# Kernel optimization log

Measured on AMD Instinct MI355X. Metric: run time of the kernel, lower is better.

The kernel has to match this reference:

```python
import jax, jax.numpy as jnp
import numpy as np

SINKHORN_ITERS = 5
EPS_CLAMP = 1e-8   # matches torch eps=1e-08 in unbalanced_optimal_transport
EPS_COS = 1e-6     # matches cosine_distance eps
EPS_DIV = 1e-6     # matches weighted_ref / rigid transform eps


def setup_inputs() -> dict:
    key = jax.random.key(0)
    k0, k1, k2, k3 = jax.random.split(key, 4)
    B, D, M, N = 32, 512, 1024, 1024
    return {
        "src_embedding": jax.random.normal(k0, (B, D, M), dtype=jnp.float32),
        "tgt_embedding": jax.random.normal(k1, (B, D, N), dtype=jnp.float32),
        "src": jax.random.normal(k2, (B, 3, M), dtype=jnp.float32),
        "tgt": jax.random.normal(k3, (B, 3, N), dtype=jnp.float32),
        "l": jnp.float32(1.0),    # learned scalar nn.Parameter
        "rho": jnp.float32(1.0),  # learned scalar nn.Parameter
    }


def reference(src_embedding, tgt_embedding, src, tgt, l, rho):
    # ---- batched cosine distance: C[b] = 1 - <x1, x2> / (|x1||x2|) ----
    x1 = jnp.swapaxes(src_embedding, 1, 2)  # (B, M, D)
    x2 = jnp.swapaxes(tgt_embedding, 1, 2)  # (B, N, D)
    w1 = jnp.linalg.norm(x1, axis=2, keepdims=True)  # (B, M, 1)
    w2 = jnp.linalg.norm(x2, axis=2, keepdims=True)  # (B, N, 1)
    denom = jnp.clip(w1 * jnp.swapaxes(w2, 1, 2), EPS_COS, None)
    C = 1.0 - jnp.einsum('bmd,bnd->bmn', x1, x2) / denom  # (B, M, N)

    # ---- batched unbalanced Sinkhorn (5 fixed iterations) ----
    B, M, N = C.shape
    a = jnp.float32(1.0 / M)
    b = jnp.float32(1.0 / N)
    K = jnp.exp(-C / jnp.clip(l, EPS_CLAMP, None))        # (B, M, N)
    fi = rho / jnp.clip(rho + l, EPS_CLAMP, None)
    v = jnp.full((B, N), b, dtype=C.dtype)
    u = jnp.full((B, M), a, dtype=C.dtype)
    for _ in range(SINKHORN_ITERS):
        u = (a / jnp.clip(jnp.einsum('bmn,bn->bm', K, v), EPS_CLAMP, None)) ** fi
        v = (b / jnp.clip(jnp.einsum('bmn,bm->bn', K, u), EPS_CLAMP, None)) ** fi
    P = u[:, :, None] * K * v[:, None, :]                  # transport plan (B, M, N)

    # ---- soft correspondences ----
    row = jnp.sum(P, axis=2)                               # (B, M)
    tgt_pts = jnp.swapaxes(tgt, 1, 2)                      # (B, N, 3)
    weighted_ref = jnp.einsum('bmn,bnd->bmd', P, tgt_pts) / (row[:, :, None] + EPS_DIV)

    # ---- weighted Kabsch rigid transform (batched 3x3 SVD) ----
    a_pts = jnp.swapaxes(src, 1, 2)                        # (B, M, 3)
    w = row[:, :, None] / (jnp.sum(row, axis=1)[:, None, None] + EPS_DIV)  # (B, M, 1)
    centroid_a = jnp.sum(a_pts * w, axis=1)                # (B, 3)
    centroid_b = jnp.sum(weighted_ref * w, axis=1)         # (B, 3)
    a_c = a_pts - centroid_a[:, None, :]
    b_c = weighted_ref - centroid_b[:, None, :]
    cov = jnp.einsum('bmi,bmj->bij', a_c, b_c * w)         # (B, 3, 3)

    U, S, Vh = jnp.linalg.svd(cov, full_matrices=True)
    V = jnp.swapaxes(Vh, 1, 2)                             # torch.svd returns V, not V^T
    Ut = jnp.swapaxes(U, 1, 2)
    rot_pos = V @ Ut
    rot_neg = V.at[:, :, 2].multiply(-1.0) @ Ut            # flip last column of V
    det = jnp.linalg.det(rot_pos)[:, None, None]
    R = jnp.where(det > 0, rot_pos, rot_neg)               # (B, 3, 3)
    t = -jnp.einsum('bij,bj->bi', R, centroid_a) + centroid_b  # (B, 3)
    return R, t, P
```

## Files before the change

### kernel.cpp

```cpp
#include <hip/hip_runtime.h>
#include <math.h>

#define BB 32
#define DD 512
#define MM 1024
#define NN 1024

typedef float f32x4 __attribute__((ext_vector_type(4)));
typedef _Float16 f16x8 __attribute__((ext_vector_type(8)));


__global__ __launch_bounds__(256)
void prep_kernel(const float* __restrict__ srcE, const float* __restrict__ tgtE,
                 float* __restrict__ w1, float* __restrict__ w2,
                 float* __restrict__ v, float* __restrict__ colsum,
                 float* __restrict__ Pout)
{
    __shared__ float T[64][65];
    __shared__ float nsum[64];
    const int mc  = blockIdx.x;
    const int mat = blockIdx.y;
    const int b   = blockIdx.z;
    const int tid = threadIdx.x;
    const float* E = mat ? tgtE : srcE;
    float* w = mat ? w2 : w1;

    if (tid < 64) nsum[tid] = 0.f;
    if (mat == 0 && tid < 64) {
        const int idx = ((b << 4) + mc) * 64 + tid;
        v[idx] = 1.0f / 1024.0f;
        colsum[idx] = 0.0f;
    }

    const int m4  = (tid & 15) * 4;
    const int din = tid >> 4;
    const int m0g = mc * 64;
    const float* Eb = E + (size_t)b * (DD * MM) + m0g;

    const int row = tid >> 2;
    const int dc4 = tid & 3;
    const int Rrow = mat * 32768 + b * 1024 + m0g + row;
    char* obase = (char*)Pout + (((size_t)(Rrow >> 1)) << 12) + 2048
                + ((size_t)(Rrow & 1) << 10);

    float nacc[4] = {0.f, 0.f, 0.f, 0.f};

    for (int p = 0; p < 8; ++p) {
        const int d0 = p * 64;
        __syncthreads();
        float4 ld[4];
        #pragma unroll
        for (int s = 0; s < 4; ++s) {
            const int d = d0 + din + 16 * s;
            ld[s] = *reinterpret_cast<const float4*>(Eb + (size_t)d * MM + m4);
        }
        #pragma unroll
        for (int s = 0; s < 4; ++s) {
            nacc[0] = fmaf(ld[s].x, ld[s].x, nacc[0]);
            nacc[1] = fmaf(ld[s].y, ld[s].y, nacc[1]);
            nacc[2] = fmaf(ld[s].z, ld[s].z, nacc[2]);
            nacc[3] = fmaf(ld[s].w, ld[s].w, nacc[3]);
            *reinterpret_cast<float4*>(&T[din + 16 * s][m4]) = ld[s];
        }
        __syncthreads();
        __attribute__((aligned(16))) _Float16 h[16];
        #pragma unroll
        for (int k = 0; k < 16; ++k) h[k] = (_Float16)T[dc4 * 16 + k][row];
        *reinterpret_cast<f16x8*>(obase + (size_t)(d0 + dc4 * 16) * 2)
            = *reinterpret_cast<f16x8*>(&h[0]);
        *reinterpret_cast<f16x8*>(obase + (size_t)(d0 + dc4 * 16 + 8) * 2)
            = *reinterpret_cast<f16x8*>(&h[8]);
    }
    #pragma unroll
    for (int q = 0; q < 4; ++q) atomicAdd(&nsum[m4 + q], nacc[q]);
    __syncthreads();
    if (tid < 64) w[b * 1024 + m0g + tid] = sqrtf(nsum[tid]);
}

__global__ __launch_bounds__(256)
void gemm_kexp_kernel(const float* __restrict__ w1, const float* __restrict__ w2,
                      const float* __restrict__ lp, float* __restrict__ Kout)
{
    __shared__ _Float16 As[2][8192];
    __shared__ _Float16 Bs[2][8192];

    const int tid  = threadIdx.x;
    const int lane = tid & 63;
    const int wave = tid >> 6;
    const int m0 = blockIdx.x * 128;
    const int n0 = blockIdx.y * 128;
    const int b  = blockIdx.z;
    const int wm = (wave & 1) * 64;
    const int wn = (wave >> 1) * 64;
    const int m16  = lane & 15;
    const int quad = lane >> 4;

    const char* pbase = (const char*)Kout;
    const char* srcA[4]; const char* srcB[4];
    #pragma unroll
    for (int c = 0; c < 4; ++c) {
        const int idx  = (wave * 4 + c) * 64 + lane;
        const int m    = idx >> 3;
        const int kg   = idx & 7;
        const int colb = ((kg ^ (m & 7)) << 4);
        const int Ra = b * 1024 + m0 + m;
        srcA[c] = pbase + (((size_t)(Ra >> 1)) << 12) + 2048
                + ((size_t)(Ra & 1) << 10) + colb;
        const int Rb = 32768 + b * 1024 + n0 + m;
        srcB[c] = pbase + (((size_t)(Rb >> 1)) << 12) + 2048
                + ((size_t)(Rb & 1) << 10) + colb;
    }

    f32x4 acc[4][4];
    #pragma unroll
    for (int i = 0; i < 4; ++i)
        #pragma unroll
        for (int j = 0; j < 4; ++j)
            acc[i][j] = (f32x4){0.f, 0.f, 0.f, 0.f};

    auto stage = [&](int buf, int kt_) {
        const int kb = kt_ * 128;
        #pragma unroll
        for (int c = 0; c < 4; ++c) {
            __builtin_amdgcn_global_load_lds(
                (const __attribute__((address_space(1))) unsigned int*)(srcA[c] + kb),
                (__attribute__((address_space(3))) unsigned int*)&As[buf][(wave * 4 + c) * 512],
                16, 0, 0);
            __builtin_amdgcn_global_load_lds(
                (const __attribute__((address_space(1))) unsigned int*)(srcB[c] + kb),
                (__attribute__((address_space(3))) unsigned int*)&Bs[buf][(wave * 4 + c) * 512],
                16, 0, 0);
        }
    };

    stage(0, 0);
    __syncthreads();
    int cur = 0;
    for (int kt = 0; kt < 8; ++kt) {
        if (kt < 7) stage(cur ^ 1, kt + 1);
        #pragma unroll
        for (int ks = 0; ks < 2; ++ks) {
            const int kg = ks * 4 + quad;
            f16x8 af[4], bfr[4];
            #pragma unroll
            for (int i = 0; i < 4; ++i) {
                const int rm = wm + i * 16 + m16;
                af[i]  = *reinterpret_cast<const f16x8*>(&As[cur][rm * 64 + ((kg ^ (rm & 7)) << 3)]);
                const int rn = wn + i * 16 + m16;
                bfr[i] = *reinterpret_cast<const f16x8*>(&Bs[cur][rn * 64 + ((kg ^ (rn & 7)) << 3)]);
            }
            #pragma unroll
            for (int i = 0; i < 4; ++i)
                #pragma unroll
                for (int j = 0; j < 4; ++j)
                    acc[i][j] = __builtin_amdgcn_mfma_f32_16x16x32_f16(af[i], bfr[j], acc[i][j], 0, 0, 0);
        }
        __syncthreads();
        cur ^= 1;
    }

    const float inv_l = 1.0f / fmaxf(lp[0], 1e-8f);
    float w2v[4];
    #pragma unroll
    for (int j = 0; j < 4; ++j) w2v[j] = w2[b * NN + n0 + wn + j * 16 + m16];
    unsigned short* Ls = (unsigned short*)&As[0][0];
    #pragma unroll
    for (int i = 0; i < 4; ++i) {
        #pragma unroll
        for (int r = 0; r < 4; ++r) {
            const int m = wm + i * 16 + quad * 4 + r;
            const float w1v = w1[b * MM + m0 + m];
            #pragma unroll
            for (int j = 0; j < 4; ++j) {
                const float dot = acc[i][j][r];
                const float den = fmaxf(w1v * w2v[j], 1e-6f);
                const float kv  = __expf((dot / den - 1.0f) * inv_l);
                const int n = wn + j * 16 + m16;
                const int sidx = m * 128 + ((((n >> 3) ^ (m & 7)) << 3) | (n & 7));
                Ls[sidx] = (unsigned short)fminf(fmaf(kv, 65535.0f, 0.5f), 65535.0f);
            }
        }
    }
    __syncthreads();
    const int row = tid >> 1, half = tid & 1;
    char* orow = (char*)Kout + ((size_t)(b * 1024 + m0 + row) << 12)
               + (size_t)n0 * 2 + half * 128;
    #pragma unroll
    for (int c = 0; c < 8; ++c) {
        const int g = half * 8 + c;
        const uint4 val = *reinterpret_cast<const uint4*>(
            &Ls[row * 128 + ((g ^ (row & 7)) << 3)]);
        reinterpret_cast<uint4*>(orow)[c] = val;
    }
}

__global__ __launch_bounds__(256)
void uv_fused_kernel(const float* __restrict__ Kmat, const float* __restrict__ v,
                     float* __restrict__ u, float* __restrict__ colsum,
                     const float* __restrict__ lp, const float* __restrict__ rp)
{
    const int ms = blockIdx.x;
    const int b  = blockIdx.y;
    const int wv = threadIdx.x >> 6, lane = threadIdx.x & 63;
    const float l = lp[0], rho = rp[0];
    const float fi = rho / fmaxf(rho + l, 1e-8f);
    const int m0 = ms * 32 + wv * 8;
    const int gid0 = (b << 10) + m0;

    uint4 ku[8][2];
    #pragma unroll
    for (int r = 0; r < 8; ++r) {
        const uint4* kr = (const uint4*)((const char*)Kmat + ((size_t)(gid0 + r) << 12));
        ku[r][0] = kr[lane];
        ku[r][1] = kr[64 + lane];
    }
    const float4* vb4 = (const float4*)(v + (b << 10));
    float4 vv[4];
    vv[0] = vb4[2 * lane];       vv[1] = vb4[2 * lane + 1];
    vv[2] = vb4[128 + 2 * lane]; vv[3] = vb4[129 + 2 * lane];

    float s[8];
    #pragma unroll
    for (int r = 0; r < 8; ++r) {
        float t = 0.f;
        #pragma unroll
        for (int c = 0; c < 2; ++c) {
            const uint4 q = ku[r][c];
            const float4 va = vv[2 * c], vb2 = vv[2 * c + 1];
            t = fmaf((float)(q.x & 0xffffu), va.x, t);
            t = fmaf((float)(q.x >> 16),     va.y, t);
            t = fmaf((float)(q.y & 0xffffu), va.z, t);
            t = fmaf((float)(q.y >> 16),     va.w, t);
            t = fmaf((float)(q.z & 0xffffu), vb2.x, t);
            t = fmaf((float)(q.z >> 16),     vb2.y, t);
            t = fmaf((float)(q.w & 0xffffu), vb2.z, t);
            t = fmaf((float)(q.w >> 16),     vb2.w, t);
        }
        s[r] = t;
    }
    #pragma unroll
    for (int off = 32; off > 0; off >>= 1)
        #pragma unroll
        for (int r = 0; r < 8; ++r) s[r] += __shfl_down(s[r], off);
    float um[8];
    #pragma unroll
    for (int r = 0; r < 8; ++r) {
        const float sv = __builtin_amdgcn_readfirstlane(s[r]) * (1.0f / 65535.0f);
        um[r] = __powf((1.0f / 1024.0f) / fmaxf(sv, 1e-8f), fi);
    }
    if (lane == 0) {
        float* ub = u + (b << 10);
        #pragma unroll
        for (int r = 0; r < 8; ++r) ub[m0 + r] = um[r];
    }

    float cacc[16];
    #pragma unroll
    for (int j = 0; j < 16; ++j) cacc[j] = 0.f;
    #pragma unroll
    for (int r = 0; r < 8; ++r) {
        const float umr = um[r];
        #pragma unroll
        for (int c = 0; c < 2; ++c) {
            const uint4 q = ku[r][c];
            float* cc = &cacc[8 * c];
            cc[0] = fmaf((float)(q.x & 0xffffu), umr, cc[0]);
            cc[1] = fmaf((float)(q.x >> 16),     umr, cc[1]);
            cc[2] = fmaf((float)(q.y & 0xffffu), umr, cc[2]);
            cc[3] = fmaf((float)(q.y >> 16),     umr, cc[3]);
            cc[4] = fmaf((float)(q.z & 0xffffu), umr, cc[4]);
            cc[5] = fmaf((float)(q.z >> 16),     umr, cc[5]);
            cc[6] = fmaf((float)(q.w & 0xffffu), umr, cc[6]);
            cc[7] = fmaf((float)(q.w >> 16),     umr, cc[7]);
        }
    }
    __shared__ float red[4][1024];
    *reinterpret_cast<float4*>(&red[wv][8 * lane])           = make_float4(cacc[0],  cacc[1],  cacc[2],  cacc[3]);
    *reinterpret_cast<float4*>(&red[wv][8 * lane + 4])       = make_float4(cacc[4],  cacc[5],  cacc[6],  cacc[7]);
    *reinterpret_cast<float4*>(&red[wv][512 + 8 * lane])     = make_float4(cacc[8],  cacc[9],  cacc[10], cacc[11]);
    *reinterpret_cast<float4*>(&red[wv][512 + 8 * lane + 4]) = make_float4(cacc[12], cacc[13], cacc[14], cacc[15]);
    __syncthreads();
    const int t = threadIdx.x;
    float4 s4 = *reinterpret_cast<const float4*>(&red[0][4 * t]);
    #pragma unroll
    for (int w = 1; w < 4; ++w) {
        const float4 rw = *reinterpret_cast<const float4*>(&red[w][4 * t]);
        s4.x += rw.x; s4.y += rw.y; s4.z += rw.z; s4.w += rw.w;
    }
    float* cs = colsum + (b << 10) + 4 * t;
    atomicAdd(cs + 0, s4.x);
    atomicAdd(cs + 1, s4.y);
    atomicAdd(cs + 2, s4.z);
    atomicAdd(cs + 3, s4.w);
}

__global__ __launch_bounds__(256)
void v_finalize_kernel(float* __restrict__ colsum, float* __restrict__ v,
                       const float* __restrict__ lp, const float* __restrict__ rp)
{
    const int idx = blockIdx.x * 256 + threadIdx.x;
    const float s = colsum[idx] * (1.0f / 65535.0f);
    colsum[idx] = 0.0f;
    const float l = lp[0], rho = rp[0];
    const float fi = rho / fmaxf(rho + l, 1e-8f);
    v[idx] = __powf((1.0f / 1024.0f) / fmaxf(s, 1e-8f), fi);
}

__global__ __launch_bounds__(256)
void p_pass_kernel(float* __restrict__ Kmat, const float* __restrict__ u,
                   const float* __restrict__ v, const float* __restrict__ tgt,
                   float* __restrict__ rowb, float* __restrict__ wref)
{
    const int gid  = (blockIdx.x * 256 + threadIdx.x) >> 6;
    const int lane = threadIdx.x & 63;
    const int b = gid >> 10;
    char* rowbase = (char*)Kmat + ((size_t)gid << 12);
    const uint4* kr = (const uint4*)rowbase;
    uint4 ku[2];
    ku[0] = kr[lane];
    ku[1] = kr[64 + lane];
    const float4* vb = (const float4*)(v + (b << 10));
    const float4* tb = (const float4*)(tgt + (size_t)b * 3072);
    const float um_s = u[gid] * (1.0f / 65535.0f);
    float4 vv[4], txa[4], tya[4], tza[4];
    vv[0]  = vb[2 * lane];        vv[1]  = vb[2 * lane + 1];
    vv[2]  = vb[128 + 2 * lane];  vv[3]  = vb[129 + 2 * lane];
    txa[0] = tb[2 * lane];        txa[1] = tb[2 * lane + 1];
    txa[2] = tb[128 + 2 * lane];  txa[3] = tb[129 + 2 * lane];
    tya[0] = tb[256 + 2 * lane];  tya[1] = tb[257 + 2 * lane];
    tya[2] = tb[384 + 2 * lane];  tya[3] = tb[385 + 2 * lane];
    tza[0] = tb[512 + 2 * lane];  tza[1] = tb[513 + 2 * lane];
    tza[2] = tb[640 + 2 * lane];  tza[3] = tb[641 + 2 * lane];
    asm volatile("s_waitcnt vmcnt(0)" ::: "memory");
    float4* prow = (float4*)rowbase;
    float s = 0.f, x = 0.f, y = 0.f, z = 0.f;
    #pragma unroll
    for (int c = 0; c < 2; ++c) {
        const uint4 q = ku[c];
        const float k0 = (float)(q.x & 0xffffu), k1 = (float)(q.x >> 16);
        const float k2 = (float)(q.y & 0xffffu), k3 = (float)(q.y >> 16);
        const float k4 = (float)(q.z & 0xffffu), k5 = (float)(q.z >> 16);
        const float k6 = (float)(q.w & 0xffffu), k7 = (float)(q.w >> 16);
        const float4 va = vv[2 * c], vb2 = vv[2 * c + 1];
        float4 pa, pb;
        pa.x = um_s * k0 * va.x;  pa.y = um_s * k1 * va.y;
        pa.z = um_s * k2 * va.z;  pa.w = um_s * k3 * va.w;
        pb.x = um_s * k4 * vb2.x; pb.y = um_s * k5 * vb2.y;
        pb.z = um_s * k6 * vb2.z; pb.w = um_s * k7 * vb2.w;
        prow[c * 128 + 2 * lane]     = pa;
        prow[c * 128 + 2 * lane + 1] = pb;
        s += (pa.x + pa.y) + (pa.z + pa.w) + (pb.x + pb.y) + (pb.z + pb.w);
        const float4 x0 = txa[2 * c], x1 = txa[2 * c + 1];
        const float4 y0 = tya[2 * c], y1 = tya[2 * c + 1];
        const float4 z0 = tza[2 * c], z1 = tza[2 * c + 1];
        x = fmaf(pa.x, x0.x, x); x = fmaf(pa.y, x0.y, x);
        x = fmaf(pa.z, x0.z, x); x = fmaf(pa.w, x0.w, x);
        x = fmaf(pb.x, x1.x, x); x = fmaf(pb.y, x1.y, x);
        x = fmaf(pb.z, x1.z, x); x = fmaf(pb.w, x1.w, x);
        y = fmaf(pa.x, y0.x, y); y = fmaf(pa.y, y0.y, y);
        y = fmaf(pa.z, y0.z, y); y = fmaf(pa.w, y0.w, y);
        y = fmaf(pb.x, y1.x, y); y = fmaf(pb.y, y1.y, y);
        y = fmaf(pb.z, y1.z, y); y = fmaf(pb.w, y1.w, y);
        z = fmaf(pa.x, z0.x, z); z = fmaf(pa.y, z0.y, z);
        z = fmaf(pa.z, z0.z, z); z = fmaf(pa.w, z0.w, z);
        z = fmaf(pb.x, z1.x, z); z = fmaf(pb.y, z1.y, z);
        z = fmaf(pb.z, z1.z, z); z = fmaf(pb.w, z1.w, z);
    }
    #pragma unroll
    for (int off = 32; off > 0; off >>= 1) {
        s += __shfl_down(s, off);
        x += __shfl_down(x, off);
        y += __shfl_down(y, off);
        z += __shfl_down(z, off);
    }
    if (lane == 0) {
        rowb[gid] = s;
        const float inv = 1.0f / (s + 1e-6f);
        wref[gid * 3 + 0] = x * inv;
        wref[gid * 3 + 1] = y * inv;
        wref[gid * 3 + 2] = z * inv;
    }
}

__device__ __forceinline__ float block_reduce_sum(float x, float* lds4, int wv, int lane)
{
    #pragma unroll
    for (int off = 32; off > 0; off >>= 1) x += __shfl_down(x, off);
    __syncthreads();
    if (lane == 0) lds4[wv] = x;
    __syncthreads();
    return (lds4[0] + lds4[1]) + (lds4[2] + lds4[3]);
}

__global__ __launch_bounds__(256)
void kabsch_stats_kernel(const float* __restrict__ rowb, const float* __restrict__ wref,
                         const float* __restrict__ src, float* __restrict__ cov,
                         float* __restrict__ ca, float* __restrict__ cb)
{
    __shared__ float lds4[4];
    const int b = blockIdx.x, tid = threadIdx.x;
    const int wv = tid >> 6, lane = tid & 63;
    float r[4], w[4], ax[4], ay[4], az[4], bx[4], by[4], bz[4];
    float rsum = 0.f;
    #pragma unroll
    for (int i = 0; i < 4; ++i) {
        const int m = tid + 256 * i;
        r[i] = rowb[(b << 10) + m];
        rsum += r[i];
    }
    const float total = block_reduce_sum(rsum, lds4, wv, lane);
    const float inv = 1.0f / (total + 1e-6f);
    #pragma unroll
    for (int i = 0; i < 4; ++i) {
        const int m = tid + 256 * i;
        w[i]  = r[i] * inv;
        ax[i] = src[b * 3072 + m];
        ay[i] = src[b * 3072 + 1024 + m];
        az[i] = src[b * 3072 + 2048 + m];
        bx[i] = wref[((b << 10) + m) * 3 + 0];
        by[i] = wref[((b << 10) + m) * 3 + 1];
        bz[i] = wref[((b << 10) + m) * 3 + 2];
    }
    float cax = 0, cay = 0, caz = 0, cbx = 0, cby = 0, cbz = 0;
    #pragma unroll
    for (int i = 0; i < 4; ++i) {
        cax = fmaf(ax[i], w[i], cax); cay = fmaf(ay[i], w[i], cay); caz = fmaf(az[i], w[i], caz);
        cbx = fmaf(bx[i], w[i], cbx); cby = fmaf(by[i], w[i], cby); cbz = fmaf(bz[i], w[i], cbz);
    }
    cax = block_reduce_sum(cax, lds4, wv, lane);
    cay = block_reduce_sum(cay, lds4, wv, lane);
    caz = block_reduce_sum(caz, lds4, wv, lane);
    cbx = block_reduce_sum(cbx, lds4, wv, lane);
    cby = block_reduce_sum(cby, lds4, wv, lane);
    cbz = block_reduce_sum(cbz, lds4, wv, lane);
    float c[9] = {0,0,0,0,0,0,0,0,0};
    #pragma unroll
    for (int i = 0; i < 4; ++i) {
        const float dax = ax[i] - cax, day = ay[i] - cay, daz = az[i] - caz;
        const float dbx = (bx[i] - cbx) * w[i];
        const float dby = (by[i] - cby) * w[i];
        const float dbz = (bz[i] - cbz) * w[i];
        c[0] = fmaf(dax, dbx, c[0]); c[1] = fmaf(dax, dby, c[1]); c[2] = fmaf(dax, dbz, c[2]);
        c[3] = fmaf(day, dbx, c[3]); c[4] = fmaf(day, dby, c[4]); c[5] = fmaf(day, dbz, c[5]);
        c[6] = fmaf(daz, dbx, c[6]); c[7] = fmaf(daz, dby, c[7]); c[8] = fmaf(daz, dbz, c[8]);
    }
    #pragma unroll
    for (int k = 0; k < 9; ++k) c[k] = block_reduce_sum(c[k], lds4, wv, lane);
    if (tid == 0) {
        #pragma unroll
        for (int k = 0; k < 9; ++k) cov[b * 9 + k] = c[k];
        ca[b * 3 + 0] = cax; ca[b * 3 + 1] = cay; ca[b * 3 + 2] = caz;
        cb[b * 3 + 0] = cbx; cb[b * 3 + 1] = cby; cb[b * 3 + 2] = cbz;
    }
}

__device__ __forceinline__ void jrot_d(double S[3][3], double V[3][3], int p, int q)
{
    const double apq = S[p][q];
    if (fabs(apq) < 1e-300) return;
    const double theta = (S[q][q] - S[p][p]) / (2.0 * apq);
    const double tt = copysign(1.0, theta) / (fabs(theta) + sqrt(1.0 + theta * theta));
    const double c = 1.0 / sqrt(1.0 + tt * tt);
    const double s = tt * c;
    #pragma unroll
    for (int k = 0; k < 3; ++k) {
        const double skp = S[k][p], skq = S[k][q];
        S[k][p] = c * skp - s * skq;
        S[k][q] = s * skp + c * skq;
    }
    #pragma unroll
    for (int k = 0; k < 3; ++k) {
        const double spk = S[p][k], sqk = S[q][k];
        S[p][k] = c * spk - s * sqk;
        S[q][k] = s * spk + c * sqk;
    }
    #pragma unroll
    for (int k = 0; k < 3; ++k) {
        const double vkp = V[k][p], vkq = V[k][q];
        V[k][p] = c * vkp - s * vkq;
        V[k][q] = s * vkp + c * vkq;
    }
}

__global__ __launch_bounds__(64)
void svd_kernel(const float* __restrict__ cov, const float* __restrict__ ca,
                const float* __restrict__ cb, float* __restrict__ out)
{
    const int b = threadIdx.x;
    if (b >= 32) return;
    double A[3][3];
    #pragma unroll
    for (int i = 0; i < 3; ++i)
        #pragma unroll
        for (int j = 0; j < 3; ++j)
            A[i][j] = (double)cov[b * 9 + i * 3 + j];
    double S[3][3];
    #pragma unroll
    for (int i = 0; i < 3; ++i)
        #pragma unroll
        for (int j = 0; j < 3; ++j)
            S[i][j] = A[0][i] * A[0][j] + A[1][i] * A[1][j] + A[2][i] * A[2][j];
    double V[3][3] = {{1,0,0},{0,1,0},{0,0,1}};
    for (int sweep = 0; sweep < 8; ++sweep) {
        jrot_d(S, V, 0, 1);
        jrot_d(S, V, 0, 2);
        jrot_d(S, V, 1, 2);
    }
    int o0 = 0, o1 = 1, o2 = 2;
    double e0 = S[0][0], e1 = S[1][1], e2 = S[2][2];
    double tf; int ti;
    if (e0 < e1) { tf = e0; e0 = e1; e1 = tf; ti = o0; o0 = o1; o1 = ti; }
    if (e0 < e2) { tf = e0; e0 = e2; e2 = tf; ti = o0; o0 = o2; o2 = ti; }
    if (e1 < e2) { tf = e1; e1 = e2; e2 = tf; ti = o1; o1 = o2; o2 = ti; }
    double v1[3] = {V[0][o0], V[1][o0], V[2][o0]};
    double v2[3] = {V[0][o1], V[1][o1], V[2][o1]};
    double v3[3] = {V[0][o2], V[1][o2], V[2][o2]};
    double Av1[3], Av2[3];
    #pragma unroll
    for (int i = 0; i < 3; ++i) {
        Av1[i] = A[i][0] * v1[0] + A[i][1] * v1[1] + A[i][2] * v1[2];
        Av2[i] = A[i][0] * v2[0] + A[i][1] * v2[1] + A[i][2] * v2[2];
    }
    const double n1 = sqrt(Av1[0]*Av1[0] + Av1[1]*Av1[1] + Av1[2]*Av1[2]);
    const double in1 = 1.0 / fmax(n1, 1e-300);
    double u1[3] = {Av1[0]*in1, Av1[1]*in1, Av1[2]*in1};
    const double d12 = Av2[0]*u1[0] + Av2[1]*u1[1] + Av2[2]*u1[2];
    double u2[3] = {Av2[0] - d12*u1[0], Av2[1] - d12*u1[1], Av2[2] - d12*u1[2]};
    const double n2 = sqrt(u2[0]*u2[0] + u2[1]*u2[1] + u2[2]*u2[2]);
    const double in2 = 1.0 / fmax(n2, 1e-300);
    u2[0] *= in2; u2[1] *= in2; u2[2] *= in2;
    double u3[3] = {u1[1]*u2[2] - u1[2]*u2[1],
                    u1[2]*u2[0] - u1[0]*u2[2],
                    u1[0]*u2[1] - u1[1]*u2[0]};
    double R0[3][3];
    #pragma unroll
    for (int i = 0; i < 3; ++i)
        #pragma unroll
        for (int j = 0; j < 3; ++j)
            R0[i][j] = v1[i]*u1[j] + v2[i]*u2[j] + v3[i]*u3[j];
    const double det =
        R0[0][0]*(R0[1][1]*R0[2][2] - R0[1][2]*R0[2][1])
      - R0[0][1]*(R0[1][0]*R0[2][2] - R0[1][2]*R0[2][0])
      + R0[0][2]*(R0[1][0]*R0[2][1] - R0[1][1]*R0[2][0]);
    double Rm[3][3];
    if (det > 0.0) {
        #pragma unroll
        for (int i = 0; i < 3; ++i)
            #pragma unroll
            for (int j = 0; j < 3; ++j)
                Rm[i][j] = R0[i][j];
    } else {
        #pragma unroll
        for (int i = 0; i < 3; ++i)
            #pragma unroll
            for (int j = 0; j < 3; ++j)
                Rm[i][j] = R0[i][j] - 2.0 * v3[i] * u3[j];
    }
    const double cax = (double)ca[b*3+0], cay = (double)ca[b*3+1], caz = (double)ca[b*3+2];
    #pragma unroll
    for (int i = 0; i < 3; ++i)
        #pragma unroll
        for (int j = 0; j < 3; ++j)
            out[b * 9 + i * 3 + j] = (float)Rm[i][j];
    #pragma unroll
    for (int i = 0; i < 3; ++i)
        out[288 + b * 3 + i] = (float)((double)cb[b*3+i] - (Rm[i][0]*cax + Rm[i][1]*cay + Rm[i][2]*caz));
}

extern "C" void kernel_launch(void* const* d_in, const int* in_sizes, int n_in,
                              void* d_out, int out_size, void* d_ws, size_t ws_size,
                              hipStream_t stream)
{
    const float* srcE = (const float*)d_in[0];
    const float* tgtE = (const float*)d_in[1];
    const float* src  = (const float*)d_in[2];
    const float* tgt  = (const float*)d_in[3];
    const float* lp   = (const float*)d_in[4];
    const float* rp   = (const float*)d_in[5];
    float* out  = (float*)d_out;
    float* Pout = out + 384;

    float* ws     = (float*)d_ws;
    float* w1     = ws;
    float* w2     = ws + 32768;
    float* u      = ws + 65536;
    float* v      = ws + 98304;
    float* rowb   = ws + 131072;
    float* wref   = ws + 163840;
    float* colsum = ws + 262144;
    float* cov    = ws + 294912;
    float* ca     = ws + 295200;
    float* cb     = ws + 295296;

    prep_kernel<<<dim3(16, 2, 32), 256, 0, stream>>>(srcE, tgtE, w1, w2, v, colsum, Pout);
    gemm_kexp_kernel<<<dim3(8, 8, 32), 256, 0, stream>>>(w1, w2, lp, Pout);
    for (int it = 0; it < 5; ++it) {
        uv_fused_kernel<<<dim3(32, 32), 256, 0, stream>>>(Pout, v, u, colsum, lp, rp);
        v_finalize_kernel<<<128, 256, 0, stream>>>(colsum, v, lp, rp);
    }
    p_pass_kernel<<<8192, 256, 0, stream>>>(Pout, u, v, tgt, rowb, wref);
    kabsch_stats_kernel<<<32, 256, 0, stream>>>(rowb, wref, src, cov, ca, cb);
    svd_kernel<<<1, 64, 0, stream>>>(cov, ca, cb, out);
}
```

Measured before the change: 535.4 us.

## Fuse Sinkhorn iterations and P pass into one cooperative persistent kernel

Replaces the five uv/v_finalize launch pairs and the separate P pass with one cooperative kernel of 512 blocks. Each block keeps its 64 rows of the quantized K in registers across all iterations and uses grid.sync between iterations. Column partial sums go into the unused upper half of the P output buffer, double-buffered by iteration parity. This removes repeated kernel launches and re-reads of K from memory, at the cost of heavy register pressure, grid-wide barriers, and a fallback path if cooperative launch is unavailable.

```diff
diff --git a/kernel.cpp b/kernel.cpp
--- a/kernel.cpp
+++ b/kernel.cpp
@@ -1,5 +1,8 @@
 #include <hip/hip_runtime.h>
+#include <hip/hip_cooperative_groups.h>
 #include <math.h>
+
+namespace cg = cooperative_groups;
 
 #define BB 32
 #define DD 512
@@ -9,6 +12,8 @@
 typedef float f32x4 __attribute__((ext_vector_type(4)));
 typedef _Float16 f16x8 __attribute__((ext_vector_type(8)));
 
+
+#define UPPER(base, L) ((base) + (((size_t)((L) >> 9)) << 10) + 512 + ((L) & 511))
 
 __global__ __launch_bounds__(256)
 void prep_kernel(const float* __restrict__ srcE, const float* __restrict__ tgtE,
@@ -191,6 +196,212 @@
         const uint4 val = *reinterpret_cast<const uint4*>(
             &Ls[row * 128 + ((g ^ (row & 7)) << 3)]);
         reinterpret_cast<uint4*>(orow)[c] = val;
+    }
+}
+
+__global__ __launch_bounds__(256, 2)
+void sinkhorn_p_kernel(float* __restrict__ Kmat, const float* __restrict__ tgt,
+                       float* __restrict__ rowb, float* __restrict__ wref,
+                       const float* __restrict__ lp, const float* __restrict__ rp)
+{
+    cg::grid_group grid = cg::this_grid();
+    const int blk = blockIdx.x;
+    const int b   = blk >> 4;
+    const int mc  = blk & 15;
+    const int wv  = threadIdx.x >> 6, lane = threadIdx.x & 63;
+    const float l = lp[0], rho = rp[0];
+    const float fi = rho / fmaxf(rho + l, 1e-8f);
+    const int m0   = mc * 64 + wv * 16;
+    const int gid0 = (b << 10) + m0;
+
+    uint4 ku[16][2];
+    #pragma unroll
+    for (int r = 0; r < 16; ++r) {
+        const uint4* kr = (const uint4*)((const char*)Kmat + ((size_t)(gid0 + r) << 12));
+        ku[r][0] = kr[lane];
+        ku[r][1] = kr[64 + lane];
+    }
+
+    __shared__ float red[4][1024];
+    float um[16];
+    float vvs[16];
+
+    for (int it = 0; it < 5; ++it) {
+        if (it == 0) {
+            #pragma unroll
+            for (int j = 0; j < 16; ++j) vvs[j] = 1.0f / 1024.0f;
+        } else {
+            const int X = (it - 1) & 1;
+            const int base = X * 524288 + (b << 10);
+            float sm[16];
+            #pragma unroll
+            for (int j = 0; j < 16; ++j) sm[j] = 0.f;
+            #pragma unroll
+            for (int m = 0; m < 16; ++m) {
+                const int Lb = base + m * 32768;
+                const float4 a0 = *reinterpret_cast<const float4*>(UPPER(Kmat, Lb + 8 * lane));
+                const float4 a1 = *reinterpret_cast<const float4*>(UPPER(Kmat, Lb + 8 * lane + 4));
+                const float4 a2 = *reinterpret_cast<const float4*>(UPPER(Kmat, Lb + 512 + 8 * lane));
+                const float4 a3 = *reinterpret_cast<const float4*>(UPPER(Kmat, Lb + 512 + 8 * lane + 4));
+                sm[0] += a0.x;  sm[1] += a0.y;  sm[2]  += a0.z;  sm[3]  += a0.w;
+                sm[4] += a1.x;  sm[5] += a1.y;  sm[6]  += a1.z;  sm[7]  += a1.w;
+                sm[8] += a2.x;  sm[9] += a2.y;  sm[10] += a2.z;  sm[11] += a2.w;
+                sm[12] += a3.x; sm[13] += a3.y; sm[14] += a3.z;  sm[15] += a3.w;
+            }
+            #pragma unroll
+            for (int j = 0; j < 16; ++j)
+                vvs[j] = __powf((1.0f / 1024.0f) / fmaxf(sm[j] * (1.0f / 65535.0f), 1e-8f), fi);
+        }
+
+        float s[16];
+        #pragma unroll
+        for (int r = 0; r < 16; ++r) {
+            float t = 0.f;
+            #pragma unroll
+            for (int c = 0; c < 2; ++c) {
+                const uint4 q = ku[r][c];
+                t = fmaf((float)(q.x & 0xffffu), vvs[8 * c + 0], t);
+                t = fmaf((float)(q.x >> 16),     vvs[8 * c + 1], t);
+                t = fmaf((float)(q.y & 0xffffu), vvs[8 * c + 2], t);
+                t = fmaf((float)(q.y >> 16),     vvs[8 * c + 3], t);
+                t = fmaf((float)(q.z & 0xffffu), vvs[8 * c + 4], t);
+                t = fmaf((float)(q.z >> 16),     vvs[8 * c + 5], t);
+                t = fmaf((float)(q.w & 0xffffu), vvs[8 * c + 6], t);
+                t = fmaf((float)(q.w >> 16),     vvs[8 * c + 7], t);
+            }
+            s[r] = t;
+        }
+        #pragma unroll
+        for (int off = 32; off > 0; off >>= 1)
+            #pragma unroll
+            for (int r = 0; r < 16; ++r) s[r] += __shfl_down(s[r], off);
+        #pragma unroll
+        for (int r = 0; r < 16; ++r) {
+            const float sv = __builtin_amdgcn_readfirstlane(s[r]) * (1.0f / 65535.0f);
+            um[r] = __powf((1.0f / 1024.0f) / fmaxf(sv, 1e-8f), fi);
+        }
+
+        float cacc[16];
+        #pragma unroll
+        for (int j = 0; j < 16; ++j) cacc[j] = 0.f;
+        #pragma unroll
+        for (int r = 0; r < 16; ++r) {
+            const float umr = um[r];
+            #pragma unroll
+            for (int c = 0; c < 2; ++c) {
+                const uint4 q = ku[r][c];
+                float* cc = &cacc[8 * c];
+                cc[0] = fmaf((float)(q.x & 0xffffu), umr, cc[0]);
+                cc[1] = fmaf((float)(q.x >> 16),     umr, cc[1]);
+                cc[2] = fmaf((float)(q.y & 0xffffu), umr, cc[2]);
+                cc[3] = fmaf((float)(q.y >> 16),     umr, cc[3]);
+                cc[4] = fmaf((float)(q.z & 0xffffu), umr, cc[4]);
+                cc[5] = fmaf((float)(q.z >> 16),     umr, cc[5]);
+                cc[6] = fmaf((float)(q.w & 0xffffu), umr, cc[6]);
+                cc[7] = fmaf((float)(q.w >> 16),     umr, cc[7]);
+            }
+        }
+        __syncthreads();
+        *reinterpret_cast<float4*>(&red[wv][8 * lane])           = make_float4(cacc[0],  cacc[1],  cacc[2],  cacc[3]);
+        *reinterpret_cast<float4*>(&red[wv][8 * lane + 4])       = make_float4(cacc[4],  cacc[5],  cacc[6],  cacc[7]);
+        *reinterpret_cast<float4*>(&red[wv][512 + 8 * lane])     = make_float4(cacc[8],  cacc[9],  cacc[10], cacc[11]);
+        *reinterpret_cast<float4*>(&red[wv][512 + 8 * lane + 4]) = make_float4(cacc[12], cacc[13], cacc[14], cacc[15]);
+        __syncthreads();
+        const int t = threadIdx.x;
+        float4 s4 = *reinterpret_cast<const float4*>(&red[0][4 * t]);
+        #pragma unroll
+        for (int w = 1; w < 4; ++w) {
+            const float4 rw = *reinterpret_cast<const float4*>(&red[w][4 * t]);
+            s4.x += rw.x; s4.y += rw.y; s4.z += rw.z; s4.w += rw.w;
+        }
+        const int Lw = (it & 1) * 524288 + mc * 32768 + (b << 10) + 4 * t;
+        *reinterpret_cast<float4*>(UPPER(Kmat, Lw)) = s4;
+        __threadfence();
+        grid.sync();
+    }
+
+    {
+        const int base = (b << 10);
+        float sm[16];
+        #pragma unroll
+        for (int j = 0; j < 16; ++j) sm[j] = 0.f;
+        #pragma unroll
+        for (int m = 0; m < 16; ++m) {
+            const int Lb = base + m * 32768;
+            const float4 a0 = *reinterpret_cast<const float4*>(UPPER(Kmat, Lb + 8 * lane));
+            const float4 a1 = *reinterpret_cast<const float4*>(UPPER(Kmat, Lb + 8 * lane + 4));
+            const float4 a2 = *reinterpret_cast<const float4*>(UPPER(Kmat, Lb + 512 + 8 * lane));
+            const float4 a3 = *reinterpret_cast<const float4*>(UPPER(Kmat, Lb + 512 + 8 * lane + 4));
+            sm[0] += a0.x;  sm[1] += a0.y;  sm[2]  += a0.z;  sm[3]  += a0.w;
+            sm[4] += a1.x;  sm[5] += a1.y;  sm[6]  += a1.z;  sm[7]  += a1.w;
+            sm[8] += a2.x;  sm[9] += a2.y;  sm[10] += a2.z;  sm[11] += a2.w;
+            sm[12] += a3.x; sm[13] += a3.y; sm[14] += a3.z;  sm[15] += a3.w;
+        }
+        #pragma unroll
+        for (int j = 0; j < 16; ++j)
+            vvs[j] = __powf((1.0f / 1024.0f) / fmaxf(sm[j] * (1.0f / 65535.0f), 1e-8f), fi);
+    }
+    grid.sync();
+
+    const float4* tb = (const float4*)(tgt + (size_t)b * 3072);
+    float4 txa[4], tya[4], tza[4];
+    txa[0] = tb[2 * lane];        txa[1] = tb[2 * lane + 1];
+    txa[2] = tb[128 + 2 * lane];  txa[3] = tb[129 + 2 * lane];
+    tya[0] = tb[256 + 2 * lane];  tya[1] = tb[257 + 2 * lane];
+    tya[2] = tb[384 + 2 * lane];  tya[3] = tb[385 + 2 * lane];
+    tza[0] = tb[512 + 2 * lane];  tza[1] = tb[513 + 2 * lane];
+    tza[2] = tb[640 + 2 * lane];  tza[3] = tb[641 + 2 * lane];
+
+    #pragma unroll
+    for (int r = 0; r < 16; ++r) {
+        float4* prow = (float4*)((char*)Kmat + ((size_t)(gid0 + r) << 12));
+        const float um_s = um[r] * (1.0f / 65535.0f);
+        float s = 0.f, x = 0.f, y = 0.f, z = 0.f;
+        #pragma unroll
+        for (int c = 0; c < 2; ++c) {
+            const uint4 q = ku[r][c];
+            float4 pa, pb;
+            pa.x = um_s * (float)(q.x & 0xffffu) * vvs[8 * c + 0];
+            pa.y = um_s * (float)(q.x >> 16)     * vvs[8 * c + 1];
+            pa.z = um_s * (float)(q.y & 0xffffu) * vvs[8 * c + 2];
+            pa.w = um_s * (float)(q.y >> 16)     * vvs[8 * c + 3];
+            pb.x = um_s * (float)(q.z & 0xffffu) * vvs[8 * c + 4];
+            pb.y = um_s * (float)(q.z >> 16)     * vvs[8 * c + 5];
+            pb.z = um_s * (float)(q.w & 0xffffu) * vvs[8 * c + 6];
+            pb.w = um_s * (float)(q.w >> 16)     * vvs[8 * c + 7];
+            prow[c * 128 + 2 * lane]     = pa;
+            prow[c * 128 + 2 * lane + 1] = pb;
+            s += (pa.x + pa.y) + (pa.z + pa.w) + (pb.x + pb.y) + (pb.z + pb.w);
+            const float4 x0 = txa[2 * c], x1 = txa[2 * c + 1];
+            const float4 y0 = tya[2 * c], y1 = tya[2 * c + 1];
+            const float4 z0 = tza[2 * c], z1 = tza[2 * c + 1];
+            x = fmaf(pa.x, x0.x, x); x = fmaf(pa.y, x0.y, x);
+            x = fmaf(pa.z, x0.z, x); x = fmaf(pa.w, x0.w, x);
+            x = fmaf(pb.x, x1.x, x); x = fmaf(pb.y, x1.y, x);
+            x = fmaf(pb.z, x1.z, x); x = fmaf(pb.w, x1.w, x);
+            y = fmaf(pa.x, y0.x, y); y = fmaf(pa.y, y0.y, y);
+            y = fmaf(pa.z, y0.z, y); y = fmaf(pa.w, y0.w, y);
+            y = fmaf(pb.x, y1.x, y); y = fmaf(pb.y, y1.y, y);
+            y = fmaf(pb.z, y1.z, y); y = fmaf(pb.w, y1.w, y);
+            z = fmaf(pa.x, z0.x, z); z = fmaf(pa.y, z0.y, z);
+            z = fmaf(pa.z, z0.z, z); z = fmaf(pa.w, z0.w, z);
+            z = fmaf(pb.x, z1.x, z); z = fmaf(pb.y, z1.y, z);
+            z = fmaf(pb.z, z1.z, z); z = fmaf(pb.w, z1.w, z);
+        }
+        #pragma unroll
+        for (int off = 32; off > 0; off >>= 1) {
+            s += __shfl_down(s, off);
+            x += __shfl_down(x, off);
+            y += __shfl_down(y, off);
+            z += __shfl_down(z, off);
+        }
+        if (lane == 0) {
+            rowb[gid0 + r] = s;
+            const float inv = 1.0f / (s + 1e-6f);
+            wref[(gid0 + r) * 3 + 0] = x * inv;
+            wref[(gid0 + r) * 3 + 1] = y * inv;
+            wref[(gid0 + r) * 3 + 2] = z * inv;
+        }
     }
 }
 
@@ -594,11 +805,43 @@
 
     prep_kernel<<<dim3(16, 2, 32), 256, 0, stream>>>(srcE, tgtE, w1, w2, v, colsum, Pout);
     gemm_kexp_kernel<<<dim3(8, 8, 32), 256, 0, stream>>>(w1, w2, lp, Pout);
-    for (int it = 0; it < 5; ++it) {
-        uv_fused_kernel<<<dim3(32, 32), 256, 0, stream>>>(Pout, v, u, colsum, lp, rp);
-        v_finalize_kernel<<<128, 256, 0, stream>>>(colsum, v, lp, rp);
-    }
-    p_pass_kernel<<<8192, 256, 0, stream>>>(Pout, u, v, tgt, rowb, wref);
+
+    static int coop_state = -1;
+    if (coop_state < 0) {
+        int nb = 0, mp = 0, dev = 0;
+        (void)hipGetDevice(&dev);
+        hipError_t e1 = hipOccupancyMaxActiveBlocksPerMultiprocessor(
+            &nb, reinterpret_cast<const void*>(sinkhorn_p_kernel), 256, 0);
+        hipError_t e2 = hipDeviceGetAttribute(
+            &mp, hipDeviceAttributeMultiprocessorCount, dev);
+        coop_state = (e1 == hipSuccess && e2 == hipSuccess && nb * mp >= 512) ? 1 : 0;
+        (void)hipGetLastError();
+    }
+
+    bool coop_done = false;
+    if (coop_state == 1) {
+        void* kargs[] = {
+            (void*)&Pout, (void*)&tgt, (void*)&rowb, (void*)&wref,
+            (void*)&lp, (void*)&rp
+        };
+        hipError_t e = hipLaunchCooperativeKernel(
+            reinterpret_cast<const void*>(sinkhorn_p_kernel),
+            dim3(512), dim3(256), kargs, 0, stream);
+        if (e == hipSuccess) {
+            coop_done = true;
+        } else {
+            (void)hipGetLastError();
+            coop_state = 0;
+        }
+    }
+    if (!coop_done) {
+        for (int it = 0; it < 5; ++it) {
+            uv_fused_kernel<<<dim3(32, 32), 256, 0, stream>>>(Pout, v, u, colsum, lp, rp);
+            v_finalize_kernel<<<128, 256, 0, stream>>>(colsum, v, lp, rp);
+        }
+        p_pass_kernel<<<8192, 256, 0, stream>>>(Pout, u, v, tgt, rowb, wref);
+    }
+
     kabsch_stats_kernel<<<32, 256, 0, stream>>>(rowb, wref, src, cov, ca, cb);
     svd_kernel<<<1, 64, 0, stream>>>(cov, ca, cb, out);
 }
```

Measured after the change: 538.9 us. About the same (+0.7%).

## Replace colsum atomics and v-finalize launches with per-block partials reduced in next iteration

Applied to the files above, without the earlier changes.

Each Sinkhorn iteration block now writes its column partial sums to a double-buffered scratch region in the unused upper half of the output P buffer instead of using atomicAdd into colsum. The next iteration reduces those 32 partials per column in-kernel and computes v itself, which removes four v_finalize launches and the atomics. The cost is that every block redundantly reads 32x1024 partials and recomputes pow for all columns, and the scratch must stay clear of K data that p_pass still reads.

```diff
diff --git a/kernel.cpp b/kernel.cpp
--- a/kernel.cpp
+++ b/kernel.cpp
@@ -10,10 +10,13 @@
 typedef _Float16 f16x8 __attribute__((ext_vector_type(8)));
 
 
+__device__ __forceinline__ float* upper_ptr(float* base, int L) {
+    return base + (((size_t)(L >> 9)) << 10) + 512 + (L & 511);
+}
+
 __global__ __launch_bounds__(256)
 void prep_kernel(const float* __restrict__ srcE, const float* __restrict__ tgtE,
                  float* __restrict__ w1, float* __restrict__ w2,
-                 float* __restrict__ v, float* __restrict__ colsum,
                  float* __restrict__ Pout)
 {
     __shared__ float T[64][65];
@@ -26,11 +29,6 @@
     float* w = mat ? w2 : w1;
 
     if (tid < 64) nsum[tid] = 0.f;
-    if (mat == 0 && tid < 64) {
-        const int idx = ((b << 4) + mc) * 64 + tid;
-        v[idx] = 1.0f / 1024.0f;
-        colsum[idx] = 0.0f;
-    }
 
     const int m4  = (tid & 15) * 4;
     const int din = tid >> 4;
@@ -195,29 +193,62 @@
 }
 
 __global__ __launch_bounds__(256)
-void uv_fused_kernel(const float* __restrict__ Kmat, const float* __restrict__ v,
-                     float* __restrict__ u, float* __restrict__ colsum,
-                     const float* __restrict__ lp, const float* __restrict__ rp)
+void sink_iter_kernel(float* __restrict__ Pb, float* __restrict__ u,
+                      const float* __restrict__ lp, const float* __restrict__ rp,
+                      const int it)
 {
     const int ms = blockIdx.x;
     const int b  = blockIdx.y;
-    const int wv = threadIdx.x >> 6, lane = threadIdx.x & 63;
+    const int tid = threadIdx.x;
+    const int wv = tid >> 6, lane = tid & 63;
     const float l = lp[0], rho = rp[0];
     const float fi = rho / fmaxf(rho + l, 1e-8f);
     const int m0 = ms * 32 + wv * 8;
     const int gid0 = (b << 10) + m0;
 
+    __shared__ float red[4][1024];
+    __shared__ float vlds[1024];
+
     uint4 ku[8][2];
     #pragma unroll
     for (int r = 0; r < 8; ++r) {
-        const uint4* kr = (const uint4*)((const char*)Kmat + ((size_t)(gid0 + r) << 12));
+        const uint4* kr = (const uint4*)((const char*)Pb + ((size_t)(gid0 + r) << 12));
         ku[r][0] = kr[lane];
         ku[r][1] = kr[64 + lane];
     }
-    const float4* vb4 = (const float4*)(v + (b << 10));
+
     float4 vv[4];
-    vv[0] = vb4[2 * lane];       vv[1] = vb4[2 * lane + 1];
-    vv[2] = vb4[128 + 2 * lane]; vv[3] = vb4[129 + 2 * lane];
+    if (it == 0) {
+        const float iv = 1.0f / 1024.0f;
+        vv[0] = vv[1] = vv[2] = vv[3] = make_float4(iv, iv, iv, iv);
+    } else {
+        const int X = (it - 1) & 1;
+        float4 a = make_float4(0.f, 0.f, 0.f, 0.f);
+        #pragma unroll
+        for (int i = 0; i < 8; ++i) {
+            const int msv = wv * 8 + i;
+            const float4 p = *reinterpret_cast<const float4*>(
+                upper_ptr(Pb, X * 1048576 + msv * 32768 + (b << 10) + 4 * tid));
+            a.x += p.x; a.y += p.y; a.z += p.z; a.w += p.w;
+        }
+        *reinterpret_cast<float4*>(&red[wv][4 * tid]) = a;
+        __syncthreads();
+        float4 s4 = *reinterpret_cast<const float4*>(&red[0][4 * tid]);
+        #pragma unroll
+        for (int w = 1; w < 4; ++w) {
+            const float4 rw = *reinterpret_cast<const float4*>(&red[w][4 * tid]);
+            s4.x += rw.x; s4.y += rw.y; s4.z += rw.z; s4.w += rw.w;
+        }
+        vlds[4 * tid + 0] = __powf((1.0f / 1024.0f) / fmaxf(s4.x * (1.0f / 65535.0f), 1e-8f), fi);
+        vlds[4 * tid + 1] = __powf((1.0f / 1024.0f) / fmaxf(s4.y * (1.0f / 65535.0f), 1e-8f), fi);
+        vlds[4 * tid + 2] = __powf((1.0f / 1024.0f) / fmaxf(s4.z * (1.0f / 65535.0f), 1e-8f), fi);
+        vlds[4 * tid + 3] = __powf((1.0f / 1024.0f) / fmaxf(s4.w * (1.0f / 65535.0f), 1e-8f), fi);
+        __syncthreads();
+        vv[0] = *reinterpret_cast<const float4*>(&vlds[8 * lane]);
+        vv[1] = *reinterpret_cast<const float4*>(&vlds[8 * lane + 4]);
+        vv[2] = *reinterpret_cast<const float4*>(&vlds[512 + 8 * lane]);
+        vv[3] = *reinterpret_cast<const float4*>(&vlds[512 + 8 * lane + 4]);
+    }
 
     float s[8];
     #pragma unroll
@@ -274,36 +305,34 @@
             cc[7] = fmaf((float)(q.w >> 16),     umr, cc[7]);
         }
     }
-    __shared__ float red[4][1024];
+    __syncthreads();
     *reinterpret_cast<float4*>(&red[wv][8 * lane])           = make_float4(cacc[0],  cacc[1],  cacc[2],  cacc[3]);
     *reinterpret_cast<float4*>(&red[wv][8 * lane + 4])       = make_float4(cacc[4],  cacc[5],  cacc[6],  cacc[7]);
     *reinterpret_cast<float4*>(&red[wv][512 + 8 * lane])     = make_float4(cacc[8],  cacc[9],  cacc[10], cacc[11]);
     *reinterpret_cast<float4*>(&red[wv][512 + 8 * lane + 4]) = make_float4(cacc[12], cacc[13], cacc[14], cacc[15]);
     __syncthreads();
-    const int t = threadIdx.x;
-    float4 s4 = *reinterpret_cast<const float4*>(&red[0][4 * t]);
+    float4 s4 = *reinterpret_cast<const float4*>(&red[0][4 * tid]);
     #pragma unroll
     for (int w = 1; w < 4; ++w) {
-        const float4 rw = *reinterpret_cast<const float4*>(&red[w][4 * t]);
+        const float4 rw = *reinterpret_cast<const float4*>(&red[w][4 * tid]);
         s4.x += rw.x; s4.y += rw.y; s4.z += rw.z; s4.w += rw.w;
     }
-    float* cs = colsum + (b << 10) + 4 * t;
-    atomicAdd(cs + 0, s4.x);
-    atomicAdd(cs + 1, s4.y);
-    atomicAdd(cs + 2, s4.z);
-    atomicAdd(cs + 3, s4.w);
+    *reinterpret_cast<float4*>(
+        upper_ptr(Pb, (it & 1) * 1048576 + ms * 32768 + (b << 10) + 4 * tid)) = s4;
 }
 
 __global__ __launch_bounds__(256)
-void v_finalize_kernel(float* __restrict__ colsum, float* __restrict__ v,
-                       const float* __restrict__ lp, const float* __restrict__ rp)
-{
-    const int idx = blockIdx.x * 256 + threadIdx.x;
-    const float s = colsum[idx] * (1.0f / 65535.0f);
-    colsum[idx] = 0.0f;
+void v_final_kernel(float* __restrict__ Pb, float* __restrict__ v,
+                    const float* __restrict__ lp, const float* __restrict__ rp)
+{
+    const int t = blockIdx.x * 256 + threadIdx.x;
     const float l = lp[0], rho = rp[0];
     const float fi = rho / fmaxf(rho + l, 1e-8f);
-    v[idx] = __powf((1.0f / 1024.0f) / fmaxf(s, 1e-8f), fi);
+    float s = 0.f;
+    #pragma unroll
+    for (int ms = 0; ms < 32; ++ms)
+        s += *upper_ptr(Pb, ms * 32768 + t);
+    v[t] = __powf((1.0f / 1024.0f) / fmaxf(s * (1.0f / 65535.0f), 1e-8f), fi);
 }
 
 __global__ __launch_bounds__(256)
@@ -580,24 +609,22 @@
     float* out  = (float*)d_out;
     float* Pout = out + 384;
 
-    float* ws     = (float*)d_ws;
-    float* w1     = ws;
-    float* w2     = ws + 32768;
-    float* u      = ws + 65536;
-    float* v      = ws + 98304;
-    float* rowb   = ws + 131072;
-    float* wref   = ws + 163840;
-    float* colsum = ws + 262144;
-    float* cov    = ws + 294912;
-    float* ca     = ws + 295200;
-    float* cb     = ws + 295296;
-
-    prep_kernel<<<dim3(16, 2, 32), 256, 0, stream>>>(srcE, tgtE, w1, w2, v, colsum, Pout);
+    float* ws   = (float*)d_ws;
+    float* w1   = ws;
+    float* w2   = ws + 32768;
+    float* u    = ws + 65536;
+    float* v    = ws + 98304;
+    float* rowb = ws + 131072;
+    float* wref = ws + 163840;
+    float* cov  = ws + 262144;
+    float* ca   = ws + 262432;
+    float* cb   = ws + 262528;
+
+    prep_kernel<<<dim3(16, 2, 32), 256, 0, stream>>>(srcE, tgtE, w1, w2, Pout);
     gemm_kexp_kernel<<<dim3(8, 8, 32), 256, 0, stream>>>(w1, w2, lp, Pout);
-    for (int it = 0; it < 5; ++it) {
-        uv_fused_kernel<<<dim3(32, 32), 256, 0, stream>>>(Pout, v, u, colsum, lp, rp);
-        v_finalize_kernel<<<128, 256, 0, stream>>>(colsum, v, lp, rp);
-    }
+    for (int it = 0; it < 5; ++it)
+        sink_iter_kernel<<<dim3(32, 32), 256, 0, stream>>>(Pout, u, lp, rp, it);
+    v_final_kernel<<<128, 256, 0, stream>>>(Pout, v, lp, rp);
     p_pass_kernel<<<8192, 256, 0, stream>>>(Pout, u, v, tgt, rowb, wref);
     kabsch_stats_kernel<<<32, 256, 0, stream>>>(rowb, wref, src, cov, ca, cb);
     svd_kernel<<<1, 64, 0, stream>>>(cov, ca, cb, out);
```

After: 516.7 us. 3.5% less time.
